# Kernel tuning notes

Hardware: AMD Instinct MI355X
Metric: run time of the kernel (lower is better)

Reference implementation:

```python
import jax, jax.numpy as jnp
import numpy as np

N_NODES = 100000
N_EDGES = 1600000
N_FEAT = 128
HIDDEN = 128
N_GRAPHS = 100


def setup_inputs() -> dict:
    key = jax.random.key(0)
    ks = jax.random.split(key, 12)
    glorot = lambda k, fi, fo: jax.random.normal(k, (fo, fi), jnp.float32) * (1.0 / np.sqrt(fi))
    x = jax.random.normal(ks[0], (N_NODES, N_FEAT), jnp.float32)
    edge_index = jax.random.randint(ks[1], (2, N_EDGES), 0, N_NODES, jnp.int64)
    batch = jnp.sort(jax.random.randint(ks[2], (N_NODES,), 0, N_GRAPHS, jnp.int64))
    return {
        "x": x,
        "edge_index": edge_index,
        "batch": batch,
        "W1": glorot(ks[3], N_FEAT, HIDDEN), "b1": jnp.zeros((HIDDEN,), jnp.float32),
        "W2": glorot(ks[4], HIDDEN, HIDDEN), "b2": jnp.zeros((HIDDEN,), jnp.float32),
        "W3": glorot(ks[5], HIDDEN, HIDDEN), "b3": jnp.zeros((HIDDEN,), jnp.float32),
        "W4": glorot(ks[6], HIDDEN, HIDDEN), "b4": jnp.zeros((HIDDEN,), jnp.float32),
    }


def _aggregate(x, edge_index):
    # GIN aggregation with eps=0: (1+eps)*x_i + sum_{j in N(i)} x_j
    src, dst = edge_index[0], edge_index[1]
    agg = jax.ops.segment_sum(x[src], dst, num_segments=N_NODES)
    return x + agg


def _mlp(h, Wa, ba, Wb, bb):
    h = jax.nn.relu(h @ Wa.T + ba)
    return jax.nn.relu(h @ Wb.T + bb)


def reference(x, edge_index, batch, W1, b1, W2, b2, W3, b3, W4, b4):
    # conv1: GINConv(MLP1), then extra relu (no-op after MLP's relu), dropout in eval = identity
    h = _mlp(_aggregate(x, edge_index), W1, b1, W2, b2)
    # conv2: GINConv(MLP2), then relu
    h = _mlp(_aggregate(h, edge_index), W3, b3, W4, b4)
    # global mean pool over graphs
    sums = jax.ops.segment_sum(h, batch, num_segments=N_GRAPHS)
    counts = jax.ops.segment_sum(jnp.ones((h.shape[0],), h.dtype), batch, num_segments=N_GRAPHS)
    x_pool = sums / jnp.maximum(counts, 1.0)[:, None]
    return (x_pool, h)
```

## Files before the change

### kernel.cpp

```cpp
#include <hip/hip_runtime.h>

#define N_NODES  100000
#define N_EDGES  1600000
#define NF       128
#define N_GRAPHS 100
#define NBKT     196
#define BKT_SHIFT 9
#define CAP      12288
#define EPB      4096
#define EB_GRID  391

typedef __attribute__((ext_vector_type(8))) short bf16x8;
typedef __attribute__((ext_vector_type(4))) float f32x4;
typedef unsigned int uint32;

__device__ __forceinline__ unsigned short f2bf(float f) {
    union { float f; uint32 u; } x; x.f = f;
    return (unsigned short)((x.u + 0x7fffu + ((x.u >> 16) & 1u)) >> 16);
}
__device__ __forceinline__ uint32 pack2bf(float a, float b) {
    union { float f; uint32 u; } x, y; x.f = a; y.f = b;
    uint32 lo = (x.u + 0x7fffu + ((x.u >> 16) & 1u)) >> 16;
    uint32 hi = (y.u + 0x7fffu + ((y.u >> 16) & 1u)) & 0xffff0000u;
    return lo | hi;
}

__global__ __launch_bounds__(256) void prep(const float4* __restrict__ x,
                                            const float4* __restrict__ w1,
                                            const float4* __restrict__ w2,
                                            const float4* __restrict__ w3,
                                            const float4* __restrict__ w4,
                                            uint4* __restrict__ xb, uint4* __restrict__ wb,
                                            int* __restrict__ cur, float* __restrict__ sums) {
    int bid = blockIdx.x, t = threadIdx.x;
    if (bid < 6250) {
        int i = bid * 256 + t;
        float4 a = x[i * 2], b = x[i * 2 + 1];
        uint4 o;
        o.x = pack2bf(a.x, a.y); o.y = pack2bf(a.z, a.w);
        o.z = pack2bf(b.x, b.y); o.w = pack2bf(b.z, b.w);
        xb[i] = o;
    } else if (bid < 6282) {
        int i = (bid - 6250) * 256 + t;
        int wi = i >> 11, li = i & 2047;
        const float4* s = (wi == 0) ? w1 : (wi == 1) ? w2 : (wi == 2) ? w3 : w4;
        float4 a = s[li * 2], b = s[li * 2 + 1];
        uint4 o;
        o.x = pack2bf(a.x, a.y); o.y = pack2bf(a.z, a.w);
        o.z = pack2bf(b.x, b.y); o.w = pack2bf(b.z, b.w);
        wb[i] = o;
    } else {
        int idx = (bid - 6282) * 256 + t;
        for (int i = idx; i < N_GRAPHS * NF; i += 4096) sums[i] = 0.f;
        if (idx < NBKT) cur[idx] = 0;
    }
}

__global__ __launch_bounds__(256) void bscatter(const int* __restrict__ src,
                                                const int* __restrict__ dst,
                                                int* __restrict__ cur,
                                                uint32* __restrict__ ebuf) {
    __shared__ int lh[NBKT], lbase[NBKT];
    int t = threadIdx.x;
    if (t < NBKT) lh[t] = 0;
    __syncthreads();
    int e0 = blockIdx.x * EPB;
    int d[16];
    #pragma unroll
    for (int i = 0; i < 16; ++i) {
        int e = e0 + i * 256 + t;
        d[i] = -1;
        if (e < N_EDGES) { d[i] = dst[e]; atomicAdd(&lh[d[i] >> BKT_SHIFT], 1); }
    }
    __syncthreads();
    if (t < NBKT) { lbase[t] = t * CAP + atomicAdd(&cur[t], lh[t]); lh[t] = 0; }
    __syncthreads();
    #pragma unroll
    for (int i = 0; i < 16; ++i) {
        int e = e0 + i * 256 + t;
        if (e < N_EDGES) {
            int b = d[i] >> BKT_SHIFT;
            int off = atomicAdd(&lh[b], 1);
            ebuf[lbase[b] + off] = ((uint32)(d[i] & 511) << 17) | (uint32)src[e];
        }
    }
}

__global__ __launch_bounds__(512) void bfine(const uint32* __restrict__ ebuf,
                                             const int* __restrict__ cur,
                                             int* __restrict__ rowptr,
                                             int* __restrict__ rowend,
                                             int* __restrict__ csr) {
    __shared__ int deg[512], off[512];
    int t = threadIdx.x;
    int bkt = blockIdx.x;
    int beg = bkt * CAP;
    int end = beg + cur[bkt];
    deg[t] = 0;
    __syncthreads();
    for (int e = beg + t; e < end; e += 512)
        atomicAdd(&deg[ebuf[e] >> 17], 1);
    __syncthreads();
    int d = deg[t];
    off[t] = d;
    __syncthreads();
    for (int o = 1; o < 512; o <<= 1) {
        int x = (t >= o) ? off[t - o] : 0;
        __syncthreads();
        off[t] += x;
        __syncthreads();
    }
    int ex = off[t] - d;
    int node = (bkt << BKT_SHIFT) + t;
    if (node < N_NODES) { rowptr[node] = beg + ex; rowend[node] = beg + ex + d; }
    __syncthreads();
    off[t] = ex;
    __syncthreads();
    for (int e = beg + t; e < end; e += 512) {
        uint32 u = ebuf[e];
        int pos = atomicAdd(&off[u >> 17], 1);
        csr[beg + pos] = (int)(u & 0x1FFFFu);
    }
}

__global__ __launch_bounds__(256) void gather_agg_bf16(const uint4* __restrict__ x,
                                                       const int* __restrict__ rowptr,
                                                       const int* __restrict__ rowend,
                                                       const int* __restrict__ csr,
                                                       uint4* __restrict__ out) {
    int idx = blockIdx.x * 256 + threadIdx.x;
    int node = idx >> 4, c = idx & 15;
    int beg = rowptr[node], end = rowend[node];

    float acc[8];
    {
        uint4 v = x[node * 16 + c];
        uint32 u[4] = {v.x, v.y, v.z, v.w};
        #pragma unroll
        for (int i = 0; i < 4; ++i) {
            union { uint32 b; float f; } lo, hi;
            lo.b = u[i] << 16; hi.b = u[i] & 0xffff0000u;
            acc[2 * i] = lo.f; acc[2 * i + 1] = hi.f;
        }
    }
    for (int e = beg; e < end; ++e) {
        int s = csr[e];
        uint4 v = x[s * 16 + c];
        uint32 u[4] = {v.x, v.y, v.z, v.w};
        #pragma unroll
        for (int i = 0; i < 4; ++i) {
            union { uint32 b; float f; } lo, hi;
            lo.b = u[i] << 16; hi.b = u[i] & 0xffff0000u;
            acc[2 * i] += lo.f; acc[2 * i + 1] += hi.f;
        }
    }
    uint4 o;
    o.x = pack2bf(acc[0], acc[1]); o.y = pack2bf(acc[2], acc[3]);
    o.z = pack2bf(acc[4], acc[5]); o.w = pack2bf(acc[6], acc[7]);
    out[node * 16 + c] = o;
}

template <bool F32OUT>
__global__ __launch_bounds__(256, 4) void mlp_mfma(const unsigned short* __restrict__ A,
                                                   const unsigned short* __restrict__ Wa,
                                                   const float* __restrict__ ba,
                                                   const unsigned short* __restrict__ Wb,
                                                   const float* __restrict__ bb,
                                                   void* __restrict__ Cout, int M) {
    __shared__ unsigned short Mid[128 * 136];
    int tid  = threadIdx.x;
    int row0 = blockIdx.x * 128;
    int wv = tid >> 6, l = tid & 63, lm = l & 15, q = l >> 4;

    const unsigned short* pa0 = A + (size_t)min(row0 + wv * 32 + lm,      M - 1) * NF;
    const unsigned short* pa1 = A + (size_t)min(row0 + wv * 32 + 16 + lm, M - 1) * NF;
    const unsigned short* pwa = Wa + lm * NF;
    const unsigned short* pwb = Wb + lm * NF;

    f32x4 acc[2][8];
    #pragma unroll
    for (int i = 0; i < 2; ++i)
        #pragma unroll
        for (int j = 0; j < 8; ++j) acc[i][j] = (f32x4){0.f, 0.f, 0.f, 0.f};

    #pragma unroll
    for (int ks = 0; ks < 4; ++ks) {
        int ko = ks * 32 + q * 8;
        bf16x8 a0 = *(const bf16x8*)(pa0 + ko);
        bf16x8 a1 = *(const bf16x8*)(pa1 + ko);
        #pragma unroll
        for (int ct = 0; ct < 8; ++ct) {
            bf16x8 b = *(const bf16x8*)(pwa + ct * 16 * NF + ko);
            acc[0][ct] = __builtin_amdgcn_mfma_f32_16x16x32_bf16(a0, b, acc[0][ct], 0, 0, 0);
            acc[1][ct] = __builtin_amdgcn_mfma_f32_16x16x32_bf16(a1, b, acc[1][ct], 0, 0, 0);
        }
    }

    #pragma unroll
    for (int rt = 0; rt < 2; ++rt)
        #pragma unroll
        for (int ct = 0; ct < 8; ++ct) {
            int col = ct * 16 + lm;
            float bv = ba[col];
            #pragma unroll
            for (int r = 0; r < 4; ++r) {
                int rr = wv * 32 + rt * 16 + q * 4 + r;
                Mid[rr * 136 + col] = f2bf(fmaxf(acc[rt][ct][r] + bv, 0.f));
            }
        }
    __syncthreads();

    #pragma unroll
    for (int i = 0; i < 2; ++i)
        #pragma unroll
        for (int j = 0; j < 8; ++j) acc[i][j] = (f32x4){0.f, 0.f, 0.f, 0.f};

    const unsigned short* pm0 = &Mid[(wv * 32 + lm) * 136];
    const unsigned short* pm1 = &Mid[(wv * 32 + 16 + lm) * 136];
    #pragma unroll
    for (int ks = 0; ks < 4; ++ks) {
        int ko = ks * 32 + q * 8;
        bf16x8 a0 = *(const bf16x8*)(pm0 + ko);
        bf16x8 a1 = *(const bf16x8*)(pm1 + ko);
        #pragma unroll
        for (int ct = 0; ct < 8; ++ct) {
            bf16x8 b = *(const bf16x8*)(pwb + ct * 16 * NF + ko);
            acc[0][ct] = __builtin_amdgcn_mfma_f32_16x16x32_bf16(a0, b, acc[0][ct], 0, 0, 0);
            acc[1][ct] = __builtin_amdgcn_mfma_f32_16x16x32_bf16(a1, b, acc[1][ct], 0, 0, 0);
        }
    }

    #pragma unroll
    for (int rt = 0; rt < 2; ++rt)
        #pragma unroll
        for (int ct = 0; ct < 8; ++ct) {
            int col = ct * 16 + lm;
            float bv = bb[col];
            #pragma unroll
            for (int r = 0; r < 4; ++r) {
                int row = row0 + wv * 32 + rt * 16 + q * 4 + r;
                if (row < M) {
                    float v = fmaxf(acc[rt][ct][r] + bv, 0.f);
                    if (F32OUT) ((float*)Cout)[(size_t)row * NF + col] = v;
                    else ((unsigned short*)Cout)[(size_t)row * NF + col] = f2bf(v);
                }
            }
        }
}

__global__ __launch_bounds__(256) void pool_sum2(const float* __restrict__ h,
                                                 const int* __restrict__ batch,
                                                 float* __restrict__ sums) {
    int t = threadIdx.x;
    int f = t & 127, seg = t >> 7;
    int n0 = blockIdx.x * 128 + seg * 64;
    if (n0 >= N_NODES) return;
    int n1 = min(n0 + 64, N_NODES);
    int cur = batch[n0];
    float acc = 0.f;
    for (int n = n0; n < n1; ++n) {
        int g = batch[n];
        if (g != cur) {
            atomicAdd(&sums[cur * NF + f], acc);
            acc = 0.f; cur = g;
        }
        acc += h[(size_t)n * NF + f];
    }
    atomicAdd(&sums[cur * NF + f], acc);
}

__global__ __launch_bounds__(256) void pool_div2(const float* __restrict__ sums,
                                                 const int* __restrict__ batch,
                                                 float* __restrict__ out) {
    int i = blockIdx.x * 256 + threadIdx.x;
    if (i >= N_GRAPHS * NF) return;
    int g = i >> 7;
    int lo = 0, hi = N_NODES;
    while (lo < hi) { int m = (lo + hi) >> 1; if (batch[m] < g) lo = m + 1; else hi = m; }
    int lo2 = lo, hi2 = N_NODES;
    while (lo2 < hi2) { int m = (lo2 + hi2) >> 1; if (batch[m] < g + 1) lo2 = m + 1; else hi2 = m; }
    float cnt = (float)(lo2 - lo);
    out[i] = sums[i] / fmaxf(cnt, 1.f);
}

extern "C" void kernel_launch(void* const* d_in, const int* in_sizes, int n_in,
                              void* d_out, int out_size, void* d_ws, size_t ws_size,
                              hipStream_t stream) {
    const float* x     = (const float*)d_in[0];
    const int*   ei    = (const int*)d_in[1];
    const int*   batch = (const int*)d_in[2];
    const float* W1 = (const float*)d_in[3];  const float* b1 = (const float*)d_in[4];
    const float* W2 = (const float*)d_in[5];  const float* b2 = (const float*)d_in[6];
    const float* W3 = (const float*)d_in[7];  const float* b3 = (const float*)d_in[8];
    const float* W4 = (const float*)d_in[9];  const float* b4 = (const float*)d_in[10];
    const int* src = ei;
    const int* dst = ei + N_EDGES;

    float* out   = (float*)d_out;
    float* h_out = out + N_GRAPHS * NF;

    const size_t NE = (size_t)N_NODES * NF;
    unsigned short* xb = (unsigned short*)d_ws;
    unsigned short* t0 = xb + NE;
    unsigned short* t1 = t0 + NE;
    unsigned short* Wb = t1 + NE;
    int*    rowptr = (int*)(Wb + 4 * NF * NF);
    int*    rowend = rowptr + N_NODES;
    int*    csr    = rowend + N_NODES;
    uint32* ebuf   = (uint32*)(csr + NBKT * CAP);
    int*    curp   = (int*)(ebuf + NBKT * CAP);
    float*  sums   = (float*)(curp + NBKT);

    const int gather_blocks = N_NODES * 16 / 256;
    const int gemm_blocks   = (N_NODES + 127) / 128;

    prep<<<6250 + 32 + 16, 256, 0, stream>>>((const float4*)x,
                                             (const float4*)W1, (const float4*)W2,
                                             (const float4*)W3, (const float4*)W4,
                                             (uint4*)xb, (uint4*)Wb, curp, sums);

    bscatter<<<EB_GRID, 256, 0, stream>>>(src, dst, curp, ebuf);
    bfine<<<NBKT, 512, 0, stream>>>(ebuf, curp, rowptr, rowend, csr);

    gather_agg_bf16<<<gather_blocks, 256, 0, stream>>>((const uint4*)xb, rowptr, rowend, csr, (uint4*)t0);
    mlp_mfma<false><<<gemm_blocks, 256, 0, stream>>>(t0, Wb + 0 * NF * NF, b1,
                                                     Wb + 1 * NF * NF, b2, t1, N_NODES);

    gather_agg_bf16<<<gather_blocks, 256, 0, stream>>>((const uint4*)t1, rowptr, rowend, csr, (uint4*)t0);
    mlp_mfma<true ><<<gemm_blocks, 256, 0, stream>>>(t0, Wb + 2 * NF * NF, b3,
                                                     Wb + 3 * NF * NF, b4, h_out, N_NODES);

    pool_sum2<<<(N_NODES + 127) / 128, 256, 0, stream>>>(h_out, batch, sums);
    pool_div2<<<(N_GRAPHS * NF + 255) / 256, 256, 0, stream>>>(sums, batch, out);
}
```

Before: 430.6 us.

## Gather neighbours with a full wave per node and use smaller CSR buckets

```diff
diff --git a/kernel.cpp b/kernel.cpp
--- a/kernel.cpp
+++ b/kernel.cpp
@@ -4,9 +4,9 @@
 #define N_EDGES  1600000
 #define NF       128
 #define N_GRAPHS 100
-#define NBKT     196
-#define BKT_SHIFT 9
-#define CAP      12288
+#define NBKT     391
+#define BKT_SHIFT 8
+#define CAP      6144
 #define EPB      4096
 #define EB_GRID  391
 
@@ -23,6 +23,15 @@
     uint32 lo = (x.u + 0x7fffu + ((x.u >> 16) & 1u)) >> 16;
     uint32 hi = (y.u + 0x7fffu + ((y.u >> 16) & 1u)) & 0xffff0000u;
     return lo | hi;
+}
+__device__ __forceinline__ void add_bf8(float* acc, uint4 v) {
+    uint32 u[4] = {v.x, v.y, v.z, v.w};
+    #pragma unroll
+    for (int i = 0; i < 4; ++i) {
+        union { uint32 b; float f; } lo, hi;
+        lo.b = u[i] << 16; hi.b = u[i] & 0xffff0000u;
+        acc[2 * i] += lo.f; acc[2 * i + 1] += hi.f;
+    }
 }
 
 __global__ __launch_bounds__(256) void prep(const float4* __restrict__ x,
@@ -56,7 +65,7 @@
     }
 }
 
-__global__ __launch_bounds__(256) void bscatter(const int* __restrict__ src,
+__global__ __launch_bounds__(512) void bscatter(const int* __restrict__ src,
                                                 const int* __restrict__ dst,
                                                 int* __restrict__ cur,
                                                 uint32* __restrict__ ebuf) {
@@ -65,10 +74,10 @@
     if (t < NBKT) lh[t] = 0;
     __syncthreads();
     int e0 = blockIdx.x * EPB;
-    int d[16];
-    #pragma unroll
-    for (int i = 0; i < 16; ++i) {
-        int e = e0 + i * 256 + t;
+    int d[8];
+    #pragma unroll
+    for (int i = 0; i < 8; ++i) {
+        int e = e0 + i * 512 + t;
         d[i] = -1;
         if (e < N_EDGES) { d[i] = dst[e]; atomicAdd(&lh[d[i] >> BKT_SHIFT], 1); }
     }
@@ -76,35 +85,35 @@
     if (t < NBKT) { lbase[t] = t * CAP + atomicAdd(&cur[t], lh[t]); lh[t] = 0; }
     __syncthreads();
     #pragma unroll
-    for (int i = 0; i < 16; ++i) {
-        int e = e0 + i * 256 + t;
+    for (int i = 0; i < 8; ++i) {
+        int e = e0 + i * 512 + t;
         if (e < N_EDGES) {
             int b = d[i] >> BKT_SHIFT;
             int off = atomicAdd(&lh[b], 1);
-            ebuf[lbase[b] + off] = ((uint32)(d[i] & 511) << 17) | (uint32)src[e];
-        }
-    }
-}
-
-__global__ __launch_bounds__(512) void bfine(const uint32* __restrict__ ebuf,
+            ebuf[lbase[b] + off] = ((uint32)(d[i] & 255) << 17) | (uint32)src[e];
+        }
+    }
+}
+
+__global__ __launch_bounds__(256) void bfine(const uint32* __restrict__ ebuf,
                                              const int* __restrict__ cur,
                                              int* __restrict__ rowptr,
                                              int* __restrict__ rowend,
                                              int* __restrict__ csr) {
-    __shared__ int deg[512], off[512];
+    __shared__ int deg[256], off[256];
     int t = threadIdx.x;
     int bkt = blockIdx.x;
     int beg = bkt * CAP;
     int end = beg + cur[bkt];
     deg[t] = 0;
     __syncthreads();
-    for (int e = beg + t; e < end; e += 512)
+    for (int e = beg + t; e < end; e += 256)
         atomicAdd(&deg[ebuf[e] >> 17], 1);
     __syncthreads();
     int d = deg[t];
     off[t] = d;
     __syncthreads();
-    for (int o = 1; o < 512; o <<= 1) {
+    for (int o = 1; o < 256; o <<= 1) {
         int x = (t >= o) ? off[t - o] : 0;
         __syncthreads();
         off[t] += x;
@@ -116,7 +125,7 @@
     __syncthreads();
     off[t] = ex;
     __syncthreads();
-    for (int e = beg + t; e < end; e += 512) {
+    for (int e = beg + t; e < end; e += 256) {
         uint32 u = ebuf[e];
         int pos = atomicAdd(&off[u >> 17], 1);
         csr[beg + pos] = (int)(u & 0x1FFFFu);
@@ -128,36 +137,46 @@
                                                        const int* __restrict__ rowend,
                                                        const int* __restrict__ csr,
                                                        uint4* __restrict__ out) {
-    int idx = blockIdx.x * 256 + threadIdx.x;
-    int node = idx >> 4, c = idx & 15;
+    int gid  = blockIdx.x * 256 + threadIdx.x;
+    int node = gid >> 6;
+    int l = threadIdx.x & 63;
+    int c = l & 15;
+    int j = l >> 4;
     int beg = rowptr[node], end = rowend[node];
 
     float acc[8];
-    {
-        uint4 v = x[node * 16 + c];
-        uint32 u[4] = {v.x, v.y, v.z, v.w};
-        #pragma unroll
-        for (int i = 0; i < 4; ++i) {
-            union { uint32 b; float f; } lo, hi;
-            lo.b = u[i] << 16; hi.b = u[i] & 0xffff0000u;
-            acc[2 * i] = lo.f; acc[2 * i + 1] = hi.f;
-        }
-    }
-    for (int e = beg; e < end; ++e) {
-        int s = csr[e];
-        uint4 v = x[s * 16 + c];
-        uint32 u[4] = {v.x, v.y, v.z, v.w};
-        #pragma unroll
-        for (int i = 0; i < 4; ++i) {
-            union { uint32 b; float f; } lo, hi;
-            lo.b = u[i] << 16; hi.b = u[i] & 0xffff0000u;
-            acc[2 * i] += lo.f; acc[2 * i + 1] += hi.f;
-        }
-    }
-    uint4 o;
-    o.x = pack2bf(acc[0], acc[1]); o.y = pack2bf(acc[2], acc[3]);
-    o.z = pack2bf(acc[4], acc[5]); o.w = pack2bf(acc[6], acc[7]);
-    out[node * 16 + c] = o;
+    #pragma unroll
+    for (int i = 0; i < 8; ++i) acc[i] = 0.f;
+
+    for (int e = beg; e < end; e += 16) {
+        int s[4];
+        #pragma unroll
+        for (int k = 0; k < 4; ++k) {
+            int ee = min(e + j + 4 * k, end - 1);
+            s[k] = csr[ee];
+        }
+        uint4 v[4];
+        #pragma unroll
+        for (int k = 0; k < 4; ++k) v[k] = x[s[k] * 16 + c];
+        #pragma unroll
+        for (int k = 0; k < 4; ++k)
+            if (e + j + 4 * k < end) add_bf8(acc, v[k]);
+    }
+
+    #pragma unroll
+    for (int i = 0; i < 8; ++i) {
+        acc[i] += __shfl_xor(acc[i], 16, 64);
+        acc[i] += __shfl_xor(acc[i], 32, 64);
+    }
+
+    add_bf8(acc, x[node * 16 + c]);
+
+    if (j == 0) {
+        uint4 o;
+        o.x = pack2bf(acc[0], acc[1]); o.y = pack2bf(acc[2], acc[3]);
+        o.z = pack2bf(acc[4], acc[5]); o.w = pack2bf(acc[6], acc[7]);
+        out[node * 16 + c] = o;
+    }
 }
 
 template <bool F32OUT>
@@ -311,7 +330,7 @@
     int*    curp   = (int*)(ebuf + NBKT * CAP);
     float*  sums   = (float*)(curp + NBKT);
 
-    const int gather_blocks = N_NODES * 16 / 256;
+    const int gather_blocks = N_NODES * 64 / 256;
     const int gemm_blocks   = (N_NODES + 127) / 128;
 
     prep<<<6250 + 32 + 16, 256, 0, stream>>>((const float4*)x,
@@ -319,8 +338,8 @@
                                              (const float4*)W3, (const float4*)W4,
                                              (uint4*)xb, (uint4*)Wb, curp, sums);
 
-    bscatter<<<EB_GRID, 256, 0, stream>>>(src, dst, curp, ebuf);
-    bfine<<<NBKT, 512, 0, stream>>>(ebuf, curp, rowptr, rowend, csr);
+    bscatter<<<EB_GRID, 512, 0, stream>>>(src, dst, curp, ebuf);
+    bfine<<<NBKT, 256, 0, stream>>>(ebuf, curp, rowptr, rowend, csr);
 
     gather_agg_bf16<<<gather_blocks, 256, 0, stream>>>((const uint4*)xb, rowptr, rowend, csr, (uint4*)t0);
     mlp_mfma<false><<<gemm_blocks, 256, 0, stream>>>(t0, Wb + 0 * NF * NF, b1,
```

Measured after the change: 409.8 us. 4.8% less time.
